# Performance work log

Hardware: AMD Instinct MI355X
Metric: run time of the kernel (lower is better)

The kernel has to match this reference:

```python
import jax, jax.numpy as jnp
import numpy as np

OUT_F, IN_F = 8192, 4096
TOKENS = 512


def _unpack_int2_to_ternary(packed, alpha, dtype):
    # packed: [out_f, in_f//4] ints 0..255; 4 two-bit codes per byte.
    # code 0 -> -1, code 2 -> +1, codes 1/3 -> 0; then scale by per-row alpha.
    shifts = jnp.arange(4, dtype=packed.dtype) * 2  # [0,2,4,6]
    two_bit = (packed[:, :, None] >> shifts[None, None, :]) & 3  # [out_f, in_f//4, 4]
    two_bit = two_bit.reshape(packed.shape[0], -1)  # [out_f, in_f]
    sign = jnp.where(two_bit == 2, 1.0, jnp.where(two_bit == 0, -1.0, 0.0)).astype(dtype)
    return sign * alpha.astype(dtype)[:, None]


def setup_inputs() -> dict:
    key = jax.random.key(0)
    k1, k2, k3, k4 = jax.random.split(key, 4)
    x = jax.random.normal(k1, (TOKENS, IN_F), dtype=jnp.float32)
    weight_int2 = jax.random.randint(k2, (OUT_F, IN_F // 4), 0, 256, dtype=jnp.int32)
    alpha = jax.random.uniform(k3, (OUT_F,), dtype=jnp.float32, minval=0.01, maxval=0.05)
    bias = jax.random.normal(k4, (OUT_F,), dtype=jnp.float32) * 0.01
    return {"x": x, "weight_int2": weight_int2, "alpha": alpha, "bias": bias}


def reference(x, weight_int2, alpha, bias):
    W = _unpack_int2_to_ternary(weight_int2, alpha, x.dtype)  # [out_f, in_f]
    out = x @ W.T  # [tokens, out_f]
    return out + bias
```

## Files before the change

kernel.cpp:

```cpp
#include <hip/hip_runtime.h>
#include <hip/hip_bf16.h>

typedef unsigned int u32;
typedef unsigned short u16;

#define TOKENS 512
#define OUT_F  8192
#define IN_F   4096
#define KPACK  (IN_F / 4)
#define TMB 128
#define TNB 128
#define BKW 128
#define NWIN (IN_F / BKW)

typedef __attribute__((ext_vector_type(8))) short bf16x8;
typedef __attribute__((ext_vector_type(4))) float f32x4;
typedef __attribute__((ext_vector_type(16))) float f32x16;

__device__ __forceinline__ u32 pack_bf16x2(float a, float b) {
    __hip_bfloat162 h = __float22bfloat162_rn(make_float2(a, b));
    union { __hip_bfloat162 h2; u32 u; } cvt;
    cvt.h2 = h;
    return cvt.u;
}

__device__ __forceinline__ u32 decode_pair(u32 d) {
    u32 s = (__umul24(d, 0x808202u) & 0x06060606u) + 0x01000100u;
    return __builtin_amdgcn_perm(0x00003F80u, 0x0000BF80u, s);
}
__device__ __forceinline__ bf16x8 decode_frag(u32 w, int sh) {
    union { bf16x8 v; u32 u[4]; } c;
    c.u[0] = decode_pair((w >> (sh + 0)) & 0xFu);
    c.u[1] = decode_pair((w >> (sh + 4)) & 0xFu);
    c.u[2] = decode_pair((w >> (sh + 8)) & 0xFu);
    c.u[3] = decode_pair((w >> (sh + 12)) & 0xFu);
    return c.v;
}

__device__ __forceinline__ void async_ld16(const void* g, void* l) {
    __builtin_amdgcn_global_load_lds(
        (const __attribute__((address_space(1))) u32*)g,
        (__attribute__((address_space(3))) u32*)l, 16, 0, 0);
}

__global__ __launch_bounds__(256) void convert_x(const float* __restrict__ X,
                                                 u16* __restrict__ Xb) {
    int i = (blockIdx.x * 256 + threadIdx.x) * 8;
    float4 a = *(const float4*)(X + i);
    float4 b = *(const float4*)(X + i + 4);
    uint4 q;
    q.x = pack_bf16x2(a.x, a.y);
    q.y = pack_bf16x2(a.z, a.w);
    q.z = pack_bf16x2(b.x, b.y);
    q.w = pack_bf16x2(b.z, b.w);
    *(uint4*)(Xb + i) = q;
}

__global__ __launch_bounds__(256) void repack_w7(const u32* __restrict__ W2,
                                                 uint2* __restrict__ W7) {
    __shared__ u32 dense[128 * 32];
    const int ngrp = blockIdx.x;
    const int kc   = blockIdx.y;
    const int t = threadIdx.x;
#pragma unroll
    for (int i = 0; i < 16; ++i) {
        int id = t + 256 * i;
        int col = id >> 5, jq = id & 31;
        uint4 wv = *(const uint4*)(W2 + (size_t)(ngrp * 128 + col) * KPACK + kc * 128 + jq * 4);
        dense[col * 32 + (jq ^ (col & 31))] =
            (wv.x & 0xFFu) | ((wv.y & 0xFFu) << 8) | ((wv.z & 0xFFu) << 16) | ((wv.w & 0xFFu) << 24);
    }
    __syncthreads();
    const u16* sp = (const u16*)dense;
#pragma unroll
    for (int p = 0; p < 8; ++p) {
        int e = t + 256 * p;
        int lane = e & 63;
        int kq = (e >> 6) & 3;
        int wloc = (e >> 8) & 3;
        int nh = (e >> 10) & 1;
        int h = lane >> 5;
        int c0 = nh * 64 + (lane & 31), c1 = c0 + 32;
        int j0 = wloc * 8 + kq * 2;
        u32 x0 = sp[((c0 * 32 + (j0 ^ (c0 & 31))) << 1) | h];
        u32 x1 = sp[((c0 * 32 + ((j0 + 1) ^ (c0 & 31))) << 1) | h];
        u32 y0 = sp[((c1 * 32 + (j0 ^ (c1 & 31))) << 1) | h];
        u32 y1 = sp[((c1 * 32 + ((j0 + 1) ^ (c1 & 31))) << 1) | h];
        uint2 o;
        o.x = x0 | (x1 << 16);
        o.y = y0 | (y1 << 16);
        int w = kc * 4 + wloc;
        W7[(((size_t)(ngrp * 2 + nh) * 32 + w) * 4 + kq) * 64 + lane] = o;
    }
}

__global__ __launch_bounds__(512, 2) void ternary_gemm8(
    const u16* __restrict__ Xb,
    const uint2* __restrict__ W7,
    const float* __restrict__ alpha,
    const float* __restrict__ bias,
    float* __restrict__ Out)
{
    __shared__ u16 As[2][TMB * BKW];

    const int tid  = threadIdx.x;
    const int lane = tid & 63;
    const int wave = tid >> 6;
    const int kq = wave & 3;
    const int nh = wave >> 2;

    const int m0 = blockIdx.x * TMB;
    const int ngrp = blockIdx.y;
    const int n0 = ngrp * TNB;

    f32x16 acc[4][2];
#pragma unroll
    for (int mt = 0; mt < 4; ++mt)
#pragma unroll
        for (int nt = 0; nt < 2; ++nt)
#pragma unroll
            for (int i = 0; i < 16; ++i)
                acc[mt][nt][i] = 0.f;

    const u16* ga[4];
    u32 lbase[4];
#pragma unroll
    for (int i = 0; i < 4; ++i) {
        int rbase = wave * 16 + i * 4;
        int row = rbase + (lane >> 4);
        int cd = (lane & 15) ^ (row & 15);
        ga[i] = Xb + (size_t)(m0 + row) * IN_F + cd * 8;
        lbase[i] = rbase * BKW;
    }

    int ofsA[4][2];
#pragma unroll
    for (int mt = 0; mt < 4; ++mt)
#pragma unroll
        for (int ks = 0; ks < 2; ++ks) {
            int row = mt * 32 + (lane & 31);
            int chunk = kq * 4 + ks * 2 + (lane >> 5);
            ofsA[mt][ks] = row * BKW + ((chunk ^ (row & 15))) * 8;
        }

    const uint2* wp = W7 + ((size_t)(ngrp * 2 + nh) * NWIN * 4 + kq) * 64 + lane;

    uint2 wcur = wp[0];
    uint2 wnext = wp[256];
#pragma unroll
    for (int i = 0; i < 4; ++i) async_ld16(ga[i], &As[0][lbase[i]]);
    __syncthreads();

    for (int w = 0; w < NWIN; ++w) {
        const int buf = w & 1;
        if (w + 1 < NWIN) {
            const int koff = (w + 1) * BKW;
#pragma unroll
            for (int i = 0; i < 4; ++i)
                async_ld16(ga[i] + koff, &As[buf ^ 1][lbase[i]]);
        }
        uint2 wnn = make_uint2(0, 0);
        if (w + 2 < NWIN) wnn = wp[(size_t)(w + 2) * 256];

        const u16* ab = As[buf];
#pragma unroll
        for (int ks = 0; ks < 2; ++ks) {
            bf16x8 a0 = *(const bf16x8*)(ab + ofsA[0][ks]);
            bf16x8 a1 = *(const bf16x8*)(ab + ofsA[1][ks]);
            bf16x8 a2 = *(const bf16x8*)(ab + ofsA[2][ks]);
            bf16x8 a3 = *(const bf16x8*)(ab + ofsA[3][ks]);
            bf16x8 b0 = decode_frag(wcur.x, ks * 16);
            bf16x8 b1 = decode_frag(wcur.y, ks * 16);
            acc[0][0] = __builtin_amdgcn_mfma_f32_32x32x16_bf16(a0, b0, acc[0][0], 0, 0, 0);
            acc[1][0] = __builtin_amdgcn_mfma_f32_32x32x16_bf16(a1, b0, acc[1][0], 0, 0, 0);
            acc[2][0] = __builtin_amdgcn_mfma_f32_32x32x16_bf16(a2, b0, acc[2][0], 0, 0, 0);
            acc[3][0] = __builtin_amdgcn_mfma_f32_32x32x16_bf16(a3, b0, acc[3][0], 0, 0, 0);
            acc[0][1] = __builtin_amdgcn_mfma_f32_32x32x16_bf16(a0, b1, acc[0][1], 0, 0, 0);
            acc[1][1] = __builtin_amdgcn_mfma_f32_32x32x16_bf16(a1, b1, acc[1][1], 0, 0, 0);
            acc[2][1] = __builtin_amdgcn_mfma_f32_32x32x16_bf16(a2, b1, acc[2][1], 0, 0, 0);
            acc[3][1] = __builtin_amdgcn_mfma_f32_32x32x16_bf16(a3, b1, acc[3][1], 0, 0, 0);
        }
        wcur = wnext;
        wnext = wnn;
        __syncthreads();
    }

    f32x4* red = (f32x4*)As;
#pragma unroll 1
    for (int q = 1; q < 4; ++q) {
        if (kq == q) {
            f32x4* dst = red + nh * 2048 + lane;
#pragma unroll
            for (int mt = 0; mt < 4; ++mt)
#pragma unroll
                for (int nt = 0; nt < 2; ++nt)
#pragma unroll
                    for (int sub = 0; sub < 4; ++sub) {
                        f32x4 v = {acc[mt][nt][sub * 4 + 0], acc[mt][nt][sub * 4 + 1],
                                   acc[mt][nt][sub * 4 + 2], acc[mt][nt][sub * 4 + 3]};
                        dst[(mt * 8 + nt * 4 + sub) * 64] = v;
                    }
        }
        __syncthreads();
        if (kq == 0) {
            const f32x4* src = red + nh * 2048 + lane;
#pragma unroll
            for (int mt = 0; mt < 4; ++mt)
#pragma unroll
                for (int nt = 0; nt < 2; ++nt)
#pragma unroll
                    for (int sub = 0; sub < 4; ++sub) {
                        f32x4 v = src[(mt * 8 + nt * 4 + sub) * 64];
#pragma unroll
                        for (int i = 0; i < 4; ++i)
                            acc[mt][nt][sub * 4 + i] += v[i];
                    }
        }
        __syncthreads();
    }

    if (kq == 0) {
#pragma unroll
        for (int nt = 0; nt < 2; ++nt) {
            int ncol = n0 + nh * 64 + nt * 32 + (lane & 31);
            float av = alpha[ncol];
            float bv = bias[ncol];
#pragma unroll
            for (int mt = 0; mt < 4; ++mt) {
#pragma unroll
                for (int r = 0; r < 16; ++r) {
                    int row = m0 + mt * 32 + (r & 3) + 8 * (r >> 2) + 4 * (lane >> 5);
                    Out[(size_t)row * OUT_F + ncol] = acc[mt][nt][r] * av + bv;
                }
            }
        }
    }
}

__global__ void ternary_naive(const float* __restrict__ X, const u32* __restrict__ W2,
                              const float* __restrict__ alpha, const float* __restrict__ bias,
                              float* __restrict__ Out) {
    int o  = blockIdx.x * 64 + (threadIdx.x & 63);
    int tk = blockIdx.y * 4 + (threadIdx.x >> 6);
    const float* x = X + (size_t)tk * IN_F;
    const u32* w = W2 + (size_t)o * KPACK;
    float s = 0.f;
    for (int d = 0; d < KPACK; ++d) {
        u32 b = w[d] & 0xFFu;
        const float* xp = x + d * 4;
#pragma unroll
        for (int j = 0; j < 4; ++j) {
            u32 c = (b >> (2 * j)) & 3u;
            float wv = (c == 2u) ? 1.f : ((c == 0u) ? -1.f : 0.f);
            s += xp[j] * wv;
        }
    }
    Out[(size_t)tk * OUT_F + o] = s * alpha[o] + bias[o];
}

extern "C" void kernel_launch(void* const* d_in, const int* in_sizes, int n_in,
                              void* d_out, int out_size, void* d_ws, size_t ws_size,
                              hipStream_t stream) {
    const float* x = (const float*)d_in[0];
    const u32* w2 = (const u32*)d_in[1];
    const float* alpha = (const float*)d_in[2];
    const float* bias  = (const float*)d_in[3];
    float* out = (float*)d_out;

    const size_t xb_bytes = (size_t)TOKENS * IN_F * sizeof(u16);
    const size_t w7_bytes = (size_t)OUT_F * IN_F / 4;

    if (ws_size >= xb_bytes + w7_bytes) {
        u16* xb = (u16*)d_ws;
        uint2* w7 = (uint2*)((char*)d_ws + xb_bytes);
        convert_x<<<(TOKENS * IN_F) / (256 * 8), 256, 0, stream>>>(x, xb);
        repack_w7<<<dim3(64, 8), 256, 0, stream>>>(w2, w7);
        ternary_gemm8<<<dim3(TOKENS / TMB, OUT_F / TNB), 512, 0, stream>>>(xb, w7, alpha, bias, out);
    } else {
        ternary_naive<<<dim3(OUT_F / 64, TOKENS / 4), 256, 0, stream>>>(x, w2, alpha, bias, out);
    }
}
```

Baseline: 129.7 us.

## Deepen A-tile pipeline to four LDS buffers and stage weights through LDS

The GEMM now keeps four LDS buffers for X tiles and double-buffers the packed weights in LDS, loading both with asynchronous global-to-LDS copies. Synchronisation uses explicit vmcnt waits plus barriers, and the loop covers two K-windows per iteration. The weight repack is changed to emit 16-byte records holding two windows, so each wave issues one wide load per pair. MFMA sections are wrapped in s_setprio to favour matrix issue. The aim is to hide global load latency more deeply, but LDS use grows to about 144KB, so the two-blocks-per-CU launch bound can no longer be met.

```diff
diff --git a/kernel.cpp b/kernel.cpp
--- a/kernel.cpp
+++ b/kernel.cpp
@@ -12,6 +12,7 @@
 #define TNB 128
 #define BKW 128
 #define NWIN (IN_F / BKW)
+#define NPAIR (NWIN / 2)
 
 typedef __attribute__((ext_vector_type(8))) short bf16x8;
 typedef __attribute__((ext_vector_type(4))) float f32x4;
@@ -56,8 +57,8 @@
     *(uint4*)(Xb + i) = q;
 }
 
-__global__ __launch_bounds__(256) void repack_w7(const u32* __restrict__ W2,
-                                                 uint2* __restrict__ W7) {
+__global__ __launch_bounds__(256) void repack_w8(const u32* __restrict__ W2,
+                                                 uint4* __restrict__ W8) {
     __shared__ u32 dense[128 * 32];
     const int ngrp = blockIdx.x;
     const int kc   = blockIdx.y;
@@ -73,35 +74,41 @@
     __syncthreads();
     const u16* sp = (const u16*)dense;
 #pragma unroll
-    for (int p = 0; p < 8; ++p) {
+    for (int p = 0; p < 4; ++p) {
         int e = t + 256 * p;
         int lane = e & 63;
         int kq = (e >> 6) & 3;
-        int wloc = (e >> 8) & 3;
-        int nh = (e >> 10) & 1;
+        int wp2 = (e >> 8) & 1;
+        int nh = (e >> 9) & 1;
         int h = lane >> 5;
         int c0 = nh * 64 + (lane & 31), c1 = c0 + 32;
-        int j0 = wloc * 8 + kq * 2;
-        u32 x0 = sp[((c0 * 32 + (j0 ^ (c0 & 31))) << 1) | h];
-        u32 x1 = sp[((c0 * 32 + ((j0 + 1) ^ (c0 & 31))) << 1) | h];
-        u32 y0 = sp[((c1 * 32 + (j0 ^ (c1 & 31))) << 1) | h];
-        u32 y1 = sp[((c1 * 32 + ((j0 + 1) ^ (c1 & 31))) << 1) | h];
-        uint2 o;
-        o.x = x0 | (x1 << 16);
-        o.y = y0 | (y1 << 16);
-        int w = kc * 4 + wloc;
-        W7[(((size_t)(ngrp * 2 + nh) * 32 + w) * 4 + kq) * 64 + lane] = o;
-    }
-}
-
-__global__ __launch_bounds__(512, 2) void ternary_gemm8(
+        u32 ov[4];
+#pragma unroll
+        for (int ws = 0; ws < 2; ++ws) {
+            int wloc = wp2 * 2 + ws;
+            int j0 = wloc * 8 + kq * 2;
+            u32 x0 = sp[((c0 * 32 + (j0 ^ (c0 & 31))) << 1) | h];
+            u32 x1 = sp[((c0 * 32 + ((j0 + 1) ^ (c0 & 31))) << 1) | h];
+            u32 y0 = sp[((c1 * 32 + (j0 ^ (c1 & 31))) << 1) | h];
+            u32 y1 = sp[((c1 * 32 + ((j0 + 1) ^ (c1 & 31))) << 1) | h];
+            ov[ws * 2 + 0] = x0 | (x1 << 16);
+            ov[ws * 2 + 1] = y0 | (y1 << 16);
+        }
+        uint4 q = make_uint4(ov[0], ov[1], ov[2], ov[3]);
+        int pr = kc * 2 + wp2;
+        W8[((((size_t)(ngrp * 2 + nh) * 4 + kq) * 16) + pr) * 64 + lane] = q;
+    }
+}
+
+__global__ __launch_bounds__(512, 2) void ternary_gemm9(
     const u16* __restrict__ Xb,
-    const uint2* __restrict__ W7,
+    const uint4* __restrict__ W8,
     const float* __restrict__ alpha,
     const float* __restrict__ bias,
     float* __restrict__ Out)
 {
-    __shared__ u16 As[2][TMB * BKW];
+    __shared__ u16 As[4 * TMB * BKW];
+    __shared__ uint4 Bs[2 * 512];
 
     const int tid  = threadIdx.x;
     const int lane = tid & 63;
@@ -143,34 +150,31 @@
             ofsA[mt][ks] = row * BKW + ((chunk ^ (row & 15))) * 8;
         }
 
-    const uint2* wp = W7 + ((size_t)(ngrp * 2 + nh) * NWIN * 4 + kq) * 64 + lane;
-
-    uint2 wcur = wp[0];
-    uint2 wnext = wp[256];
-#pragma unroll
-    for (int i = 0; i < 4; ++i) async_ld16(ga[i], &As[0][lbase[i]]);
-    __syncthreads();
-
-    for (int w = 0; w < NWIN; ++w) {
-        const int buf = w & 1;
-        if (w + 1 < NWIN) {
-            const int koff = (w + 1) * BKW;
-#pragma unroll
-            for (int i = 0; i < 4; ++i)
-                async_ld16(ga[i] + koff, &As[buf ^ 1][lbase[i]]);
-        }
-        uint2 wnn = make_uint2(0, 0);
-        if (w + 2 < NWIN) wnn = wp[(size_t)(w + 2) * 256];
-
-        const u16* ab = As[buf];
+    const uint4* w8p = W8 + ((((size_t)(ngrp * 2 + nh) * 4 + kq) * 16) * 64) + lane;
+    uint4* const bsb = Bs + wave * 64;
+
+    auto issueA = [&](int w) {
+        u16* dst = As + (size_t)((w & 3) * (TMB * BKW));
+        const int koff = w * BKW;
+#pragma unroll
+        for (int i = 0; i < 4; ++i)
+            async_ld16(ga[i] + koff, dst + lbase[i]);
+    };
+    auto issueB = [&](int p) {
+        async_ld16(w8p + (size_t)p * 64, bsb + (p & 1) * 512);
+    };
+
+    auto window_compute = [&](int wmod4, u32 wx, u32 wy) {
+        const u16* ab = As + (size_t)wmod4 * (TMB * BKW);
 #pragma unroll
         for (int ks = 0; ks < 2; ++ks) {
             bf16x8 a0 = *(const bf16x8*)(ab + ofsA[0][ks]);
             bf16x8 a1 = *(const bf16x8*)(ab + ofsA[1][ks]);
             bf16x8 a2 = *(const bf16x8*)(ab + ofsA[2][ks]);
             bf16x8 a3 = *(const bf16x8*)(ab + ofsA[3][ks]);
-            bf16x8 b0 = decode_frag(wcur.x, ks * 16);
-            bf16x8 b1 = decode_frag(wcur.y, ks * 16);
+            bf16x8 b0 = decode_frag(wx, ks * 16);
+            bf16x8 b1 = decode_frag(wy, ks * 16);
+            __builtin_amdgcn_s_setprio(1);
             acc[0][0] = __builtin_amdgcn_mfma_f32_32x32x16_bf16(a0, b0, acc[0][0], 0, 0, 0);
             acc[1][0] = __builtin_amdgcn_mfma_f32_32x32x16_bf16(a1, b0, acc[1][0], 0, 0, 0);
             acc[2][0] = __builtin_amdgcn_mfma_f32_32x32x16_bf16(a2, b0, acc[2][0], 0, 0, 0);
@@ -179,11 +183,47 @@
             acc[1][1] = __builtin_amdgcn_mfma_f32_32x32x16_bf16(a1, b1, acc[1][1], 0, 0, 0);
             acc[2][1] = __builtin_amdgcn_mfma_f32_32x32x16_bf16(a2, b1, acc[2][1], 0, 0, 0);
             acc[3][1] = __builtin_amdgcn_mfma_f32_32x32x16_bf16(a3, b1, acc[3][1], 0, 0, 0);
-        }
-        wcur = wnext;
-        wnext = wnn;
-        __syncthreads();
-    }
+            __builtin_amdgcn_s_setprio(0);
+        }
+    };
+
+#define WAIT_BARRIER(N) do {                                         \
+        asm volatile("s_waitcnt vmcnt(" #N ")" ::: "memory");        \
+        __builtin_amdgcn_s_barrier();                                \
+        __builtin_amdgcn_sched_barrier(0);                           \
+    } while (0)
+
+    issueA(0);
+    issueB(0);
+    issueA(1);
+
+    uint4 bv;
+#pragma unroll 1
+    for (int p = 0; p < NPAIR - 2; ++p) {
+        const int w = 2 * p;
+        issueA(w + 2);
+        issueB(p + 1);
+        WAIT_BARRIER(9);
+        bv = *(const uint4*)(Bs + (p & 1) * 512 + wave * 64 + lane);
+        window_compute(w & 3, bv.x, bv.y);
+        issueA(w + 3);
+        WAIT_BARRIER(9);
+        window_compute((w + 1) & 3, bv.z, bv.w);
+    }
+    issueA(30);
+    issueB(15);
+    WAIT_BARRIER(9);
+    bv = *(const uint4*)(Bs + 0 * 512 + wave * 64 + lane);
+    window_compute(28 & 3, bv.x, bv.y);
+    issueA(31);
+    WAIT_BARRIER(9);
+    window_compute(29 & 3, bv.z, bv.w);
+    WAIT_BARRIER(4);
+    bv = *(const uint4*)(Bs + 1 * 512 + wave * 64 + lane);
+    window_compute(30 & 3, bv.x, bv.y);
+    WAIT_BARRIER(0);
+    window_compute(31 & 3, bv.z, bv.w);
+#undef WAIT_BARRIER
 
     f32x4* red = (f32x4*)As;
 #pragma unroll 1
@@ -224,13 +264,13 @@
         for (int nt = 0; nt < 2; ++nt) {
             int ncol = n0 + nh * 64 + nt * 32 + (lane & 31);
             float av = alpha[ncol];
-            float bv = bias[ncol];
+            float bv2 = bias[ncol];
 #pragma unroll
             for (int mt = 0; mt < 4; ++mt) {
 #pragma unroll
                 for (int r = 0; r < 16; ++r) {
                     int row = m0 + mt * 32 + (r & 3) + 8 * (r >> 2) + 4 * (lane >> 5);
-                    Out[(size_t)row * OUT_F + ncol] = acc[mt][nt][r] * av + bv;
+                    Out[(size_t)row * OUT_F + ncol] = acc[mt][nt][r] * av + bv2;
                 }
             }
         }
@@ -268,14 +308,14 @@
     float* out = (float*)d_out;
 
     const size_t xb_bytes = (size_t)TOKENS * IN_F * sizeof(u16);
-    const size_t w7_bytes = (size_t)OUT_F * IN_F / 4;
-
-    if (ws_size >= xb_bytes + w7_bytes) {
+    const size_t w8_bytes = (size_t)OUT_F * IN_F / 4;
+
+    if (ws_size >= xb_bytes + w8_bytes) {
         u16* xb = (u16*)d_ws;
-        uint2* w7 = (uint2*)((char*)d_ws + xb_bytes);
+        uint4* w8 = (uint4*)((char*)d_ws + xb_bytes);
         convert_x<<<(TOKENS * IN_F) / (256 * 8), 256, 0, stream>>>(x, xb);
-        repack_w7<<<dim3(64, 8), 256, 0, stream>>>(w2, w7);
-        ternary_gemm8<<<dim3(TOKENS / TMB, OUT_F / TNB), 512, 0, stream>>>(xb, w7, alpha, bias, out);
+        repack_w8<<<dim3(64, 8), 256, 0, stream>>>(w2, w8);
+        ternary_gemm9<<<dim3(TOKENS / TMB, OUT_F / TNB), 512, 0, stream>>>(xb, w8, alpha, bias, out);
     } else {
         ternary_naive<<<dim3(OUT_F / 64, TOKENS / 4), 256, 0, stream>>>(x, w2, alpha, bias, out);
     }
```

Result: no change. 127.7 us (-1.6%).

## Halve N tile to 64 and raise occupancy with per-window u32 weight layout

Applied to the files above, without the earlier changes.

Shrinks the GEMM N tile from 128 to 64 columns, so each wave holds 4 accumulators instead of 8, and raises the launch bound to 4 blocks per CU. The weight repack now writes a u32-per-lane layout indexed by block, kq and nh, matching the smaller tile. The grid doubles to 512 blocks, which improves load balance and latency hiding on the CUs. In exchange, each X tile is re-read from L2 twice as often, and the extra blocks increase the cost of the LDS reduction and of the A-fragment loads per MFMA.

```diff
diff --git a/kernel.cpp b/kernel.cpp
--- a/kernel.cpp
+++ b/kernel.cpp
@@ -9,7 +9,7 @@
 #define IN_F   4096
 #define KPACK  (IN_F / 4)
 #define TMB 128
-#define TNB 128
+#define TNB 64
 #define BKW 128
 #define NWIN (IN_F / BKW)
 
@@ -56,8 +56,8 @@
     *(uint4*)(Xb + i) = q;
 }
 
-__global__ __launch_bounds__(256) void repack_w7(const u32* __restrict__ W2,
-                                                 uint2* __restrict__ W7) {
+__global__ __launch_bounds__(256) void repack_w9(const u32* __restrict__ W2,
+                                                 u32* __restrict__ W9) {
     __shared__ u32 dense[128 * 32];
     const int ngrp = blockIdx.x;
     const int kc   = blockIdx.y;
@@ -73,30 +73,33 @@
     __syncthreads();
     const u16* sp = (const u16*)dense;
 #pragma unroll
-    for (int p = 0; p < 8; ++p) {
+    for (int p = 0; p < 4; ++p) {
         int e = t + 256 * p;
         int lane = e & 63;
         int kq = (e >> 6) & 3;
-        int wloc = (e >> 8) & 3;
-        int nh = (e >> 10) & 1;
+        int wp2 = (e >> 8) & 1;
+        int nho = (e >> 9) & 1;
         int h = lane >> 5;
-        int c0 = nh * 64 + (lane & 31), c1 = c0 + 32;
-        int j0 = wloc * 8 + kq * 2;
-        u32 x0 = sp[((c0 * 32 + (j0 ^ (c0 & 31))) << 1) | h];
-        u32 x1 = sp[((c0 * 32 + ((j0 + 1) ^ (c0 & 31))) << 1) | h];
-        u32 y0 = sp[((c1 * 32 + (j0 ^ (c1 & 31))) << 1) | h];
-        u32 y1 = sp[((c1 * 32 + ((j0 + 1) ^ (c1 & 31))) << 1) | h];
-        uint2 o;
-        o.x = x0 | (x1 << 16);
-        o.y = y0 | (y1 << 16);
-        int w = kc * 4 + wloc;
-        W7[(((size_t)(ngrp * 2 + nh) * 32 + w) * 4 + kq) * 64 + lane] = o;
-    }
-}
-
-__global__ __launch_bounds__(512, 2) void ternary_gemm8(
+        int c0 = nho * 64 + (lane & 31), c1 = c0 + 32;
+        int nb = ngrp * 2 + nho;
+#pragma unroll
+        for (int ws = 0; ws < 2; ++ws) {
+            int wloc = wp2 * 2 + ws;
+            int w = kc * 4 + wloc;
+            int j0 = wloc * 8 + kq * 2;
+            u32 x0 = sp[((c0 * 32 + (j0 ^ (c0 & 31))) << 1) | h];
+            u32 x1 = sp[((c0 * 32 + ((j0 + 1) ^ (c0 & 31))) << 1) | h];
+            u32 y0 = sp[((c1 * 32 + (j0 ^ (c1 & 31))) << 1) | h];
+            u32 y1 = sp[((c1 * 32 + ((j0 + 1) ^ (c1 & 31))) << 1) | h];
+            W9[((((size_t)nb * 4 + kq) * 2 + 0) * NWIN + w) * 64 + lane] = x0 | (x1 << 16);
+            W9[((((size_t)nb * 4 + kq) * 2 + 1) * NWIN + w) * 64 + lane] = y0 | (y1 << 16);
+        }
+    }
+}
+
+__global__ __launch_bounds__(512, 4) void ternary_gemm10(
     const u16* __restrict__ Xb,
-    const uint2* __restrict__ W7,
+    const u32* __restrict__ W9,
     const float* __restrict__ alpha,
     const float* __restrict__ bias,
     float* __restrict__ Out)
@@ -110,45 +113,41 @@
     const int nh = wave >> 2;
 
     const int m0 = blockIdx.x * TMB;
-    const int ngrp = blockIdx.y;
-    const int n0 = ngrp * TNB;
-
-    f32x16 acc[4][2];
+    const int nb = blockIdx.y;
+    const int n0 = nb * TNB;
+
+    f32x16 acc[4];
 #pragma unroll
     for (int mt = 0; mt < 4; ++mt)
 #pragma unroll
-        for (int nt = 0; nt < 2; ++nt)
-#pragma unroll
-            for (int i = 0; i < 16; ++i)
-                acc[mt][nt][i] = 0.f;
-
-    const u16* ga[4];
+        for (int i = 0; i < 16; ++i)
+            acc[mt][i] = 0.f;
+
+    const u16* gbase = Xb + (size_t)(m0 + wave * 16) * IN_F;
+    u32 aoff[4];
     u32 lbase[4];
 #pragma unroll
     for (int i = 0; i < 4; ++i) {
-        int rbase = wave * 16 + i * 4;
-        int row = rbase + (lane >> 4);
-        int cd = (lane & 15) ^ (row & 15);
-        ga[i] = Xb + (size_t)(m0 + row) * IN_F + cd * 8;
-        lbase[i] = rbase * BKW;
-    }
-
-    int ofsA[4][2];
-#pragma unroll
-    for (int mt = 0; mt < 4; ++mt)
-#pragma unroll
-        for (int ks = 0; ks < 2; ++ks) {
-            int row = mt * 32 + (lane & 31);
-            int chunk = kq * 4 + ks * 2 + (lane >> 5);
-            ofsA[mt][ks] = row * BKW + ((chunk ^ (row & 15))) * 8;
-        }
-
-    const uint2* wp = W7 + ((size_t)(ngrp * 2 + nh) * NWIN * 4 + kq) * 64 + lane;
-
-    uint2 wcur = wp[0];
-    uint2 wnext = wp[256];
-#pragma unroll
-    for (int i = 0; i < 4; ++i) async_ld16(ga[i], &As[0][lbase[i]]);
+        int rr = i * 4 + (lane >> 4);
+        int cd = (lane & 15) ^ (rr & 15);
+        aoff[i] = rr * IN_F + cd * 8;
+        lbase[i] = (wave * 16 + i * 4) * BKW;
+    }
+
+    u32 ofsA0[2];
+#pragma unroll
+    for (int ks = 0; ks < 2; ++ks) {
+        int row = lane & 31;
+        int chunk = kq * 4 + ks * 2 + (lane >> 5);
+        ofsA0[ks] = row * BKW + (chunk ^ (row & 15)) * 8;
+    }
+
+    const u32* wq = W9 + ((((size_t)nb * 4 + kq) * 2 + nh) * NWIN) * 64 + lane;
+
+    u32 wcur = wq[0];
+    u32 wnext = wq[64];
+#pragma unroll
+    for (int i = 0; i < 4; ++i) async_ld16(gbase + aoff[i], &As[0][lbase[i]]);
     __syncthreads();
 
     for (int w = 0; w < NWIN; ++w) {
@@ -157,28 +156,24 @@
             const int koff = (w + 1) * BKW;
 #pragma unroll
             for (int i = 0; i < 4; ++i)
-                async_ld16(ga[i] + koff, &As[buf ^ 1][lbase[i]]);
-        }
-        uint2 wnn = make_uint2(0, 0);
-        if (w + 2 < NWIN) wnn = wp[(size_t)(w + 2) * 256];
+                async_ld16(gbase + aoff[i] + koff, &As[buf ^ 1][lbase[i]]);
+        }
+        u32 wnn = 0;
+        if (w + 2 < NWIN) wnn = wq[(size_t)(w + 2) * 64];
 
         const u16* ab = As[buf];
 #pragma unroll
         for (int ks = 0; ks < 2; ++ks) {
-            bf16x8 a0 = *(const bf16x8*)(ab + ofsA[0][ks]);
-            bf16x8 a1 = *(const bf16x8*)(ab + ofsA[1][ks]);
-            bf16x8 a2 = *(const bf16x8*)(ab + ofsA[2][ks]);
-            bf16x8 a3 = *(const bf16x8*)(ab + ofsA[3][ks]);
-            bf16x8 b0 = decode_frag(wcur.x, ks * 16);
-            bf16x8 b1 = decode_frag(wcur.y, ks * 16);
-            acc[0][0] = __builtin_amdgcn_mfma_f32_32x32x16_bf16(a0, b0, acc[0][0], 0, 0, 0);
-            acc[1][0] = __builtin_amdgcn_mfma_f32_32x32x16_bf16(a1, b0, acc[1][0], 0, 0, 0);
-            acc[2][0] = __builtin_amdgcn_mfma_f32_32x32x16_bf16(a2, b0, acc[2][0], 0, 0, 0);
-            acc[3][0] = __builtin_amdgcn_mfma_f32_32x32x16_bf16(a3, b0, acc[3][0], 0, 0, 0);
-            acc[0][1] = __builtin_amdgcn_mfma_f32_32x32x16_bf16(a0, b1, acc[0][1], 0, 0, 0);
-            acc[1][1] = __builtin_amdgcn_mfma_f32_32x32x16_bf16(a1, b1, acc[1][1], 0, 0, 0);
-            acc[2][1] = __builtin_amdgcn_mfma_f32_32x32x16_bf16(a2, b1, acc[2][1], 0, 0, 0);
-            acc[3][1] = __builtin_amdgcn_mfma_f32_32x32x16_bf16(a3, b1, acc[3][1], 0, 0, 0);
+            const u16* ap = ab + ofsA0[ks];
+            bf16x8 a0 = *(const bf16x8*)(ap);
+            bf16x8 a1 = *(const bf16x8*)(ap + 4096);
+            bf16x8 a2 = *(const bf16x8*)(ap + 8192);
+            bf16x8 a3 = *(const bf16x8*)(ap + 12288);
+            bf16x8 b0 = decode_frag(wcur, ks * 16);
+            acc[0] = __builtin_amdgcn_mfma_f32_32x32x16_bf16(a0, b0, acc[0], 0, 0, 0);
+            acc[1] = __builtin_amdgcn_mfma_f32_32x32x16_bf16(a1, b0, acc[1], 0, 0, 0);
+            acc[2] = __builtin_amdgcn_mfma_f32_32x32x16_bf16(a2, b0, acc[2], 0, 0, 0);
+            acc[3] = __builtin_amdgcn_mfma_f32_32x32x16_bf16(a3, b0, acc[3], 0, 0, 0);
         }
         wcur = wnext;
         wnext = wnn;
@@ -189,49 +184,42 @@
 #pragma unroll 1
     for (int q = 1; q < 4; ++q) {
         if (kq == q) {
-            f32x4* dst = red + nh * 2048 + lane;
+            f32x4* dst = red + nh * 1024 + lane;
 #pragma unroll
             for (int mt = 0; mt < 4; ++mt)
 #pragma unroll
-                for (int nt = 0; nt < 2; ++nt)
-#pragma unroll
-                    for (int sub = 0; sub < 4; ++sub) {
-                        f32x4 v = {acc[mt][nt][sub * 4 + 0], acc[mt][nt][sub * 4 + 1],
-                                   acc[mt][nt][sub * 4 + 2], acc[mt][nt][sub * 4 + 3]};
-                        dst[(mt * 8 + nt * 4 + sub) * 64] = v;
-                    }
+                for (int sub = 0; sub < 4; ++sub) {
+                    f32x4 v = {acc[mt][sub * 4 + 0], acc[mt][sub * 4 + 1],
+                               acc[mt][sub * 4 + 2], acc[mt][sub * 4 + 3]};
+                    dst[(mt * 4 + sub) * 64] = v;
+                }
         }
         __syncthreads();
         if (kq == 0) {
-            const f32x4* src = red + nh * 2048 + lane;
+            const f32x4* src = red + nh * 1024 + lane;
 #pragma unroll
             for (int mt = 0; mt < 4; ++mt)
 #pragma unroll
-                for (int nt = 0; nt < 2; ++nt)
-#pragma unroll
-                    for (int sub = 0; sub < 4; ++sub) {
-                        f32x4 v = src[(mt * 8 + nt * 4 + sub) * 64];
-#pragma unroll
-                        for (int i = 0; i < 4; ++i)
-                            acc[mt][nt][sub * 4 + i] += v[i];
-                    }
+                for (int sub = 0; sub < 4; ++sub) {
+                    f32x4 v = src[(mt * 4 + sub) * 64];
+#pragma unroll
+                    for (int i = 0; i < 4; ++i)
+                        acc[mt][sub * 4 + i] += v[i];
+                }
         }
         __syncthreads();
     }
 
     if (kq == 0) {
-#pragma unroll
-        for (int nt = 0; nt < 2; ++nt) {
-            int ncol = n0 + nh * 64 + nt * 32 + (lane & 31);
-            float av = alpha[ncol];
-            float bv = bias[ncol];
-#pragma unroll
-            for (int mt = 0; mt < 4; ++mt) {
-#pragma unroll
-                for (int r = 0; r < 16; ++r) {
-                    int row = m0 + mt * 32 + (r & 3) + 8 * (r >> 2) + 4 * (lane >> 5);
-                    Out[(size_t)row * OUT_F + ncol] = acc[mt][nt][r] * av + bv;
-                }
+        int ncol = n0 + nh * 32 + (lane & 31);
+        float av = alpha[ncol];
+        float bv = bias[ncol];
+#pragma unroll
+        for (int mt = 0; mt < 4; ++mt) {
+#pragma unroll
+            for (int r = 0; r < 16; ++r) {
+                int row = m0 + mt * 32 + (r & 3) + 8 * (r >> 2) + 4 * (lane >> 5);
+                Out[(size_t)row * OUT_F + ncol] = acc[mt][r] * av + bv;
             }
         }
     }
@@ -268,14 +256,14 @@
     float* out = (float*)d_out;
 
     const size_t xb_bytes = (size_t)TOKENS * IN_F * sizeof(u16);
-    const size_t w7_bytes = (size_t)OUT_F * IN_F / 4;
-
-    if (ws_size >= xb_bytes + w7_bytes) {
+    const size_t w9_bytes = (size_t)OUT_F * IN_F / 4;
+
+    if (ws_size >= xb_bytes + w9_bytes) {
         u16* xb = (u16*)d_ws;
-        uint2* w7 = (uint2*)((char*)d_ws + xb_bytes);
+        u32* w9 = (u32*)((char*)d_ws + xb_bytes);
         convert_x<<<(TOKENS * IN_F) / (256 * 8), 256, 0, stream>>>(x, xb);
-        repack_w7<<<dim3(64, 8), 256, 0, stream>>>(w2, w7);
-        ternary_gemm8<<<dim3(TOKENS / TMB, OUT_F / TNB), 512, 0, stream>>>(xb, w7, alpha, bias, out);
+        repack_w9<<<dim3(64, 8), 256, 0, stream>>>(w2, w9);
+        ternary_gemm10<<<dim3(TOKENS / TMB, OUT_F / TNB), 512, 0, stream>>>(xb, w9, alpha, bias, out);
     } else {
         ternary_naive<<<dim3(OUT_F / 64, TOKENS / 4), 256, 0, stream>>>(x, w2, alpha, bias, out);
     }
```

Result: no change. 131.3 us (+1.2%).

## Deepen A/B prefetch pipeline to four LDS buffers with manual vmcnt waits

Applied to the files above, without the earlier changes.

Replaces the double-buffered main loop with a four-stage LDS ring and hand-scheduled global loads of the packed weights using inline asm. Waits on explicit vmcnt counts and uses a single barrier per window instead of a full __syncthreads after compute. This is meant to keep more memory traffic in flight and reduce synchronization stalls. It doubles LDS usage per block, which may cut blocks per CU, and relies on the compiler not inserting other vector memory ops.

```diff
diff --git a/kernel.cpp b/kernel.cpp
--- a/kernel.cpp
+++ b/kernel.cpp
@@ -42,6 +42,13 @@
         (const __attribute__((address_space(1))) u32*)g,
         (__attribute__((address_space(3))) u32*)l, 16, 0, 0);
 }
+
+__device__ __forceinline__ void async_b(const uint2* g, uint2& dst) {
+    asm volatile("global_load_dwordx2 %0, %1, off"
+                 : "=v"(dst) : "v"(g) : "memory");
+}
+
+#define VMW(N) asm volatile("s_waitcnt vmcnt(" #N ")" ::: "memory")
 
 __global__ __launch_bounds__(256) void convert_x(const float* __restrict__ X,
                                                  u16* __restrict__ Xb) {
@@ -94,14 +101,14 @@
     }
 }
 
-__global__ __launch_bounds__(512, 2) void ternary_gemm8(
+__global__ __launch_bounds__(512, 2) void ternary_gemm11(
     const u16* __restrict__ Xb,
     const uint2* __restrict__ W7,
     const float* __restrict__ alpha,
     const float* __restrict__ bias,
     float* __restrict__ Out)
 {
-    __shared__ u16 As[2][TMB * BKW];
+    __shared__ u16 As[4][TMB * BKW];
 
     const int tid  = threadIdx.x;
     const int lane = tid & 63;
@@ -145,23 +152,15 @@
 
     const uint2* wp = W7 + ((size_t)(ngrp * 2 + nh) * NWIN * 4 + kq) * 64 + lane;
 
-    uint2 wcur = wp[0];
-    uint2 wnext = wp[256];
-#pragma unroll
-    for (int i = 0; i < 4; ++i) async_ld16(ga[i], &As[0][lbase[i]]);
-    __syncthreads();
-
-    for (int w = 0; w < NWIN; ++w) {
-        const int buf = w & 1;
-        if (w + 1 < NWIN) {
-            const int koff = (w + 1) * BKW;
-#pragma unroll
-            for (int i = 0; i < 4; ++i)
-                async_ld16(ga[i] + koff, &As[buf ^ 1][lbase[i]]);
-        }
-        uint2 wnn = make_uint2(0, 0);
-        if (w + 2 < NWIN) wnn = wp[(size_t)(w + 2) * 256];
-
+    auto issueA = [&](int w) {
+        u16* d = As[w & 3];
+        const int koff = w * BKW;
+#pragma unroll
+        for (int i = 0; i < 4; ++i)
+            async_ld16(ga[i] + koff, d + lbase[i]);
+    };
+
+    auto window_compute = [&](int buf, uint2 bq) {
         const u16* ab = As[buf];
 #pragma unroll
         for (int ks = 0; ks < 2; ++ks) {
@@ -169,8 +168,8 @@
             bf16x8 a1 = *(const bf16x8*)(ab + ofsA[1][ks]);
             bf16x8 a2 = *(const bf16x8*)(ab + ofsA[2][ks]);
             bf16x8 a3 = *(const bf16x8*)(ab + ofsA[3][ks]);
-            bf16x8 b0 = decode_frag(wcur.x, ks * 16);
-            bf16x8 b1 = decode_frag(wcur.y, ks * 16);
+            bf16x8 b0 = decode_frag(bq.x, ks * 16);
+            bf16x8 b1 = decode_frag(bq.y, ks * 16);
             acc[0][0] = __builtin_amdgcn_mfma_f32_32x32x16_bf16(a0, b0, acc[0][0], 0, 0, 0);
             acc[1][0] = __builtin_amdgcn_mfma_f32_32x32x16_bf16(a1, b0, acc[1][0], 0, 0, 0);
             acc[2][0] = __builtin_amdgcn_mfma_f32_32x32x16_bf16(a2, b0, acc[2][0], 0, 0, 0);
@@ -180,10 +179,39 @@
             acc[2][1] = __builtin_amdgcn_mfma_f32_32x32x16_bf16(a2, b1, acc[2][1], 0, 0, 0);
             acc[3][1] = __builtin_amdgcn_mfma_f32_32x32x16_bf16(a3, b1, acc[3][1], 0, 0, 0);
         }
-        wcur = wnext;
-        wnext = wnn;
-        __syncthreads();
-    }
+    };
+
+    uint2 bqE, bqO;
+    async_b(wp, bqE);
+    issueA(0);
+    async_b(wp + 256, bqO);
+    issueA(1);
+
+#pragma unroll 1
+    for (int p = 0; p < (NWIN - 2) / 2; ++p) {
+        const int w = 2 * p;
+        VMW(5);
+        __builtin_amdgcn_s_barrier();
+        __builtin_amdgcn_sched_barrier(0);
+        window_compute(w & 3, bqE);
+        async_b(wp + (size_t)(w + 2) * 256, bqE);
+        issueA(w + 2);
+
+        VMW(5);
+        __builtin_amdgcn_s_barrier();
+        __builtin_amdgcn_sched_barrier(0);
+        window_compute((w + 1) & 3, bqO);
+        async_b(wp + (size_t)(w + 3) * 256, bqO);
+        issueA(w + 3);
+    }
+    VMW(5);
+    __builtin_amdgcn_s_barrier();
+    __builtin_amdgcn_sched_barrier(0);
+    window_compute(30 & 3, bqE);
+    VMW(0);
+    __builtin_amdgcn_s_barrier();
+    __builtin_amdgcn_sched_barrier(0);
+    window_compute(31 & 3, bqO);
 
     f32x4* red = (f32x4*)As;
 #pragma unroll 1
@@ -275,7 +303,7 @@
         uint2* w7 = (uint2*)((char*)d_ws + xb_bytes);
         convert_x<<<(TOKENS * IN_F) / (256 * 8), 256, 0, stream>>>(x, xb);
         repack_w7<<<dim3(64, 8), 256, 0, stream>>>(w2, w7);
-        ternary_gemm8<<<dim3(TOKENS / TMB, OUT_F / TNB), 512, 0, stream>>>(xb, w7, alpha, bias, out);
+        ternary_gemm11<<<dim3(TOKENS / TMB, OUT_F / TNB), 512, 0, stream>>>(xb, w7, alpha, bias, out);
     } else {
         ternary_naive<<<dim3(OUT_F / 64, TOKENS / 4), 256, 0, stream>>>(x, w2, alpha, bias, out);
     }
```

After: 125.2 us. 1.04x faster.
